# Kernel tuning notes

Measured on AMD Instinct MI355X. Metric: run time of the kernel, lower is better.

## Reference

```python
import jax, jax.numpy as jnp
import numpy as np

# Hypernetwork config (matches init_kwargs)
INP = 4096      # inp_size
MSK = 64        # mask_size
HID = 64        # node_hidden_size (target-net hidden)
OUT = 10        # out_size (target outputs)
L1, L2, L3 = 64, 256, 128  # hypernet trunk layers
B = 16384       # batch
WVEC = MSK * HID + HID + HID * OUT + OUT  # 4810 generated weights per sample


def _linear_params(key, fan_in, fan_out):
    # torch.nn.Linear default init: U(-1/sqrt(fan_in), 1/sqrt(fan_in))
    lim = 1.0 / np.sqrt(fan_in)
    kw, kb = jax.random.split(key)
    W = jax.random.uniform(kw, (fan_out, fan_in), minval=-lim, maxval=lim, dtype=jnp.float32)
    b = jax.random.uniform(kb, (fan_out,), minval=-lim, maxval=lim, dtype=jnp.float32)
    return W, b


def setup_inputs() -> dict:
    key = jax.random.key(0)
    ks = jax.random.split(key, 6)
    W1, b1 = _linear_params(ks[0], INP, L1)
    W2, b2 = _linear_params(ks[1], L1, L2)
    W3, b3 = _linear_params(ks[2], L2, L3)
    W4, b4 = _linear_params(ks[3], L3, WVEC)
    data = jax.random.normal(ks[4], (B, INP), dtype=jnp.float32)
    mask_idx = jnp.sort(jax.random.randint(ks[5], (B, MSK), 0, INP), axis=1)  # int indices of active features
    return dict(data=data, mask_idx=mask_idx,
                W1=W1, b1=b1, W2=W2, b2=b2, W3=W3, b3=b3, W4=W4, b4=b4)


def reference(data, mask_idx, W1, b1, W2, b2, W3, b3, W4, b4):
    b = data.shape[0]
    # Rebuild the float binary mask [B, INP] from indices (scatter ones)
    rows = jnp.arange(b)[:, None]
    mask = jnp.zeros((b, INP), dtype=data.dtype).at[rows, mask_idx].set(1.0)

    # craft_network: 4-layer MLP on the mask (dropout is identity in eval / for reference)
    h = jax.nn.relu(mask @ W1.T + b1)
    h = jax.nn.relu(h @ W2.T + b2)
    h = jax.nn.relu(h @ W3.T + b3)
    w = h @ W4.T + b4  # [B, WVEC] generated weights per sample

    # Split per-sample generated weights (same layout as InsertableNet)
    iw_end = MSK * HID
    ib_end = iw_end + HID
    ow_end = ib_end + HID * OUT
    inp_w = w[:, :iw_end].reshape(b, HID, MSK)       # [B, H, M]
    inp_b = w[:, iw_end:ib_end]                      # [B, H]
    out_w = w[:, ib_end:ow_end].reshape(b, OUT, HID) # [B, O, H]
    out_b = w[:, ow_end:]                            # [B, O]

    # Per-sample gather of masked features: data[i, mask[i]] -> [B, M]
    xm = jnp.take_along_axis(data, mask_idx, axis=1)

    # Batched tiny 2-layer MLP (replaces the per-sample Python loop)
    hid = jax.nn.relu(jnp.einsum('bhm,bm->bh', inp_w, xm) + inp_b)
    res = jnp.einsum('boh,bh->bo', out_w, hid) + out_b  # [B, OUT]
    return res
```

## Files before the change

### kernel.cpp

```cpp
#include <hip/hip_runtime.h>


typedef _Float16 f16;
typedef _Float16 f16x8 __attribute__((ext_vector_type(8)));
typedef _Float16 f16x4 __attribute__((ext_vector_type(4)));
typedef float    f32x4 __attribute__((ext_vector_type(4)));

#define NPAD 4864

__global__ __launch_bounds__(256) void k_prep(
    const float* __restrict__ W1, const float* __restrict__ W2,
    const float* __restrict__ W3, const float* __restrict__ W4,
    f16* __restrict__ W1Th, f16* __restrict__ W2h,
    f16* __restrict__ W3h, f16* __restrict__ W4s)
{
    const int tid = blockIdx.x * 256 + threadIdx.x;
    const int stride = gridDim.x * 256;
    for (int e = tid; e < 4096 * 64; e += stride) {
        int j = e >> 6, i = e & 63;
        W1Th[e] = (f16)W1[(size_t)i * 4096 + j];
    }
    for (int e = tid; e < NPAD * 128; e += stride) {
        const int j    = e & 7;
        const int lane = (e >> 3) & 63;
        const int mt   = (e >> 9) & 3;
        const int kk   = (e >> 11) & 3;
        const int c    = e >> 13;
        const int lr = lane & 15, g = lane >> 4;
        const int row = 64 * c + 16 * mt + lr;
        const int col = 32 * kk + 8 * g + j;
        W4s[e] = (row < 4810) ? (f16)W4[(size_t)row * 128 + col] : (f16)0.f;
    }
    for (int e = tid; e < 256 * 64; e += stride)  W2h[e] = (f16)W2[e];
    for (int e = tid; e < 128 * 256; e += stride) W3h[e] = (f16)W3[e];
}

__global__ __launch_bounds__(512, 2) void k_main(
    const float* __restrict__ data, const int* __restrict__ midx,
    const f16* __restrict__ W1Th, const float* __restrict__ b1,
    const f16* __restrict__ W2h, const float* __restrict__ b2,
    const f16* __restrict__ W3h, const float* __restrict__ b3,
    const f16* __restrict__ W4s, const float* __restrict__ b4,
    float* __restrict__ out)
{
    __shared__ __align__(16) char uMain[65536];
    __shared__ __align__(16) char uB[17408];
    __shared__ __align__(16) char uC[17408];
    __shared__ __align__(16) float b4_s[NPAD];
    __shared__ __align__(16) float res_s[64 * 12];

    const int t = threadIdx.x, w = t >> 6, lane = t & 63;
    const int lr = lane & 15, g = lane >> 4;
    const int sg = w >> 1, cp = w & 1;
    const int row0 = blockIdx.x * 64;
    const f32x4 zero = {0.f, 0.f, 0.f, 0.f};

    int*   idx_s = (int*)uB;
    char*  h2b   = uMain;
    char*  h1b   = uMain + 32768;
    char*  h3b   = uC;
    char*  stage = uMain;
    float* xm_s  = (float*)uB;
    float* hid_s = (float*)uC;

    const char* W4b = (const char*)W4s;
    f32x4 rS0, rS1, rS2, rS3;

    {
        const char* gp = W4b + (size_t)t * 16;
        rS0 = *(const f32x4*)(gp);
        rS1 = *(const f32x4*)(gp + 8192);
        rS2 = *(const f32x4*)(gp + 16384);
        rS3 = *(const f32x4*)(gp + 24576);
    }

    for (int e = t; e < 4096; e += 512)
        idx_s[e] = midx[(size_t)row0 * 64 + e];
    for (int i = t; i < NPAD; i += 512)
        b4_s[i] = (i < 4810) ? b4[i] : 0.f;
    __syncthreads();

    float xr[8];
    #pragma unroll
    for (int k = 0; k < 8; ++k) {
        const int e = k * 512 + t;
        xr[k] = data[(size_t)(row0 + (e >> 6)) * 4096 + idx_s[e]];
    }

    {
        const f32x4 b1v = *(const f32x4*)&b1[lr * 4];
        for (int p = 0; p < 4; ++p) {
            const int s0 = 8 * w + 2 * p, s1 = s0 + 1;
            f32x4 a0 = zero, a1 = zero;
            #pragma unroll
            for (int tt = 0; tt < 16; ++tt) {
                const int i = g * 16 + tt;
                const int c0 = idx_s[s0 * 64 + i];
                const int q0 = (i > 0) ? idx_s[s0 * 64 + i - 1] : -1;
                const int c1 = idx_s[s1 * 64 + i];
                const int q1 = (i > 0) ? idx_s[s1 * 64 + i - 1] : -1;
                const f16x4 w0 = *(const f16x4*)&W1Th[c0 * 64 + lr * 4];
                const f16x4 w1 = *(const f16x4*)&W1Th[c1 * 64 + lr * 4];
                #pragma unroll
                for (int q = 0; q < 4; ++q) {
                    a0[q] += (c0 != q0) ? (float)w0[q] : 0.f;
                    a1[q] += (c1 != q1) ? (float)w1[q] : 0.f;
                }
            }
            #pragma unroll
            for (int q = 0; q < 4; ++q) {
                a0[q] += __shfl_xor(a0[q], 16);
                a0[q] += __shfl_xor(a0[q], 32);
                a1[q] += __shfl_xor(a1[q], 16);
                a1[q] += __shfl_xor(a1[q], 32);
            }
            if (g == 0) {
                f16x4 h0, h1v;
                #pragma unroll
                for (int q = 0; q < 4; ++q) {
                    h0[q]  = (f16)fmaxf(a0[q] + b1v[q], 0.f);
                    h1v[q] = (f16)fmaxf(a1[q] + b1v[q], 0.f);
                }
                *(f16x4*)(h1b + ((s0 * 128 + lr * 8) ^ ((s0 & 7) << 4))) = h0;
                *(f16x4*)(h1b + ((s1 * 128 + lr * 8) ^ ((s1 & 7) << 4))) = h1v;
            }
        }
    }
    __syncthreads();

    {
        f16x8 a2[2][2], bh[4][2];
        #pragma unroll
        for (int mt = 0; mt < 2; ++mt)
            #pragma unroll
            for (int kk = 0; kk < 2; ++kk)
                a2[mt][kk] = *(const f16x8*)&W2h[(32 * w + 16 * mt + lr) * 64 + 32 * kk + 8 * g];
        #pragma unroll
        for (int rt = 0; rt < 4; ++rt)
            #pragma unroll
            for (int kk = 0; kk < 2; ++kk) {
                const int s = 16 * rt + lr;
                bh[rt][kk] = *(const f16x8*)(h1b + ((s * 128 + (32 * kk + 8 * g) * 2) ^ ((s & 7) << 4)));
            }

        f32x4 acc2[2][4];
        #pragma unroll
        for (int mt = 0; mt < 2; ++mt)
            #pragma unroll
            for (int rt = 0; rt < 4; ++rt) {
                acc2[mt][rt] = __builtin_amdgcn_mfma_f32_16x16x32_f16(a2[mt][0], bh[rt][0], zero, 0, 0, 0);
                acc2[mt][rt] = __builtin_amdgcn_mfma_f32_16x16x32_f16(a2[mt][1], bh[rt][1], acc2[mt][rt], 0, 0, 0);
            }

        #pragma unroll
        for (int mt = 0; mt < 2; ++mt) {
            const f32x4 bv = *(const f32x4*)&b2[32 * w + 16 * mt + 4 * g];
            #pragma unroll
            for (int rt = 0; rt < 4; ++rt) {
                const int s = 16 * rt + lr;
                f16x4 hv;
                #pragma unroll
                for (int q = 0; q < 4; ++q)
                    hv[q] = (f16)fmaxf(acc2[mt][rt][q] + bv[q], 0.f);
                *(f16x4*)(h2b + ((s * 512 + (32 * w + 16 * mt + 4 * g) * 2) ^ ((s & 7) << 4))) = hv;
            }
        }
    }
    __syncthreads();

    {
        f32x4 acc3[4] = {zero, zero, zero, zero};
        #pragma unroll 2
        for (int kk = 0; kk < 8; ++kk) {
            const f16x8 a3 = *(const f16x8*)&W3h[(16 * w + lr) * 256 + 32 * kk + 8 * g];
            #pragma unroll
            for (int rt = 0; rt < 4; ++rt) {
                const int s = 16 * rt + lr;
                const f16x8 bb = *(const f16x8*)(h2b + ((s * 512 + (32 * kk + 8 * g) * 2) ^ ((s & 7) << 4)));
                acc3[rt] = __builtin_amdgcn_mfma_f32_16x16x32_f16(a3, bb, acc3[rt], 0, 0, 0);
            }
        }
        const f32x4 bv3 = *(const f32x4*)&b3[16 * w + 4 * g];
        #pragma unroll
        for (int rt = 0; rt < 4; ++rt) {
            const int s = 16 * rt + lr;
            f16x4 hv;
            #pragma unroll
            for (int q = 0; q < 4; ++q)
                hv[q] = (f16)fmaxf(acc3[rt][q] + bv3[q], 0.f);
            *(f16x4*)(h3b + ((s * 256 + (16 * w + 4 * g) * 2) ^ ((s & 7) << 4))) = hv;
        }
    }
    __syncthreads();

    {
        char* lp = stage + t * 16;
        *(f32x4*)(lp)         = rS0;
        *(f32x4*)(lp + 8192)  = rS1;
        *(f32x4*)(lp + 16384) = rS2;
        *(f32x4*)(lp + 24576) = rS3;
    }
    {
        const char* gp = W4b + 32768 + (size_t)t * 16;
        rS0 = *(const f32x4*)(gp);
        rS1 = *(const f32x4*)(gp + 8192);
        rS2 = *(const f32x4*)(gp + 16384);
        rS3 = *(const f32x4*)(gp + 24576);
    }
    #pragma unroll
    for (int k = 0; k < 8; ++k) {
        const int e = k * 512 + t;
        xm_s[(e >> 6) * 68 + (e & 63)] = xr[k];
    }
    const int s = 16 * sg + lr;
    f16x8 bfrag[4];
    #pragma unroll
    for (int kk = 0; kk < 4; ++kk)
        bfrag[kk] = *(const f16x8*)(h3b + ((s * 256 + (32 * kk + 8 * g) * 2) ^ ((s & 7) << 4)));
    __syncthreads();

    f32x4 xmr[4];
    #pragma unroll
    for (int mt = 0; mt < 4; ++mt)
        xmr[mt] = *(const f32x4*)&xm_s[s * 68 + 16 * mt + 4 * g];
    f32x4 hidr[4];

    for (int tp = 0; tp < 38; ++tp) {
        const char* pb = stage + (tp & 1) * 32768;

        if (tp < 32) {
            const int c = 2 * tp + cp;
            const char* cb = pb + (c & 1) * 16384;
            f32x4 acc[4] = {zero, zero, zero, zero};
            #pragma unroll
            for (int kk = 0; kk < 4; ++kk) {
                f16x8 af[4];
                #pragma unroll
                for (int mt = 0; mt < 4; ++mt)
                    af[mt] = *(const f16x8*)(cb + kk * 4096 + mt * 1024 + lane * 16);
                #pragma unroll
                for (int mt = 0; mt < 4; ++mt)
                    acc[mt] = __builtin_amdgcn_mfma_f32_16x16x32_f16(af[mt], bfrag[kk], acc[mt], 0, 0, 0);
            }
            float sum = 0.f;
            #pragma unroll
            for (int mt = 0; mt < 4; ++mt) {
                const f32x4 bv = *(const f32x4*)&b4_s[64 * c + 16 * mt + 4 * g];
                #pragma unroll
                for (int q = 0; q < 4; ++q)
                    sum += (acc[mt][q] + bv[q]) * xmr[mt][q];
            }
            sum += __shfl_xor(sum, 16);
            sum += __shfl_xor(sum, 32);
            if (g == 0) hid_s[s * 68 + c] = sum;
        } else if (tp == 32) {
            f32x4 accb[2] = {zero, zero};
            #pragma unroll
            for (int kk = 0; kk < 4; ++kk) {
                f16x8 af[2];
                #pragma unroll
                for (int i = 0; i < 2; ++i)
                    af[i] = *(const f16x8*)(pb + kk * 4096 + (2 * cp + i) * 1024 + lane * 16);
                #pragma unroll
                for (int i = 0; i < 2; ++i)
                    accb[i] = __builtin_amdgcn_mfma_f32_16x16x32_f16(af[i], bfrag[kk], accb[i], 0, 0, 0);
            }
            #pragma unroll
            for (int i = 0; i < 2; ++i) {
                const int hb = 16 * (2 * cp + i) + 4 * g;
                f32x4 hv = *(const f32x4*)&hid_s[s * 68 + hb];
                const f32x4 bv = *(const f32x4*)&b4_s[4096 + hb];
                #pragma unroll
                for (int q = 0; q < 4; ++q)
                    hv[q] = fmaxf(hv[q] + accb[i][q] + bv[q], 0.f);
                *(f32x4*)&hid_s[s * 68 + hb] = hv;
            }
            __syncthreads();
            #pragma unroll
            for (int mt = 0; mt < 4; ++mt)
                hidr[mt] = *(const f32x4*)&hid_s[s * 68 + 16 * mt + 4 * g];
            if (cp == 0) {
                const char* cb = pb + 16384;
                f32x4 acc[4] = {zero, zero, zero, zero};
                #pragma unroll
                for (int kk = 0; kk < 4; ++kk) {
                    f16x8 af[4];
                    #pragma unroll
                    for (int mt = 0; mt < 4; ++mt)
                        af[mt] = *(const f16x8*)(cb + kk * 4096 + mt * 1024 + lane * 16);
                    #pragma unroll
                    for (int mt = 0; mt < 4; ++mt)
                        acc[mt] = __builtin_amdgcn_mfma_f32_16x16x32_f16(af[mt], bfrag[kk], acc[mt], 0, 0, 0);
                }
                float sum = 0.f;
                #pragma unroll
                for (int mt = 0; mt < 4; ++mt) {
                    const f32x4 bv = *(const f32x4*)&b4_s[4160 + 16 * mt + 4 * g];
                    #pragma unroll
                    for (int q = 0; q < 4; ++q)
                        sum += (acc[mt][q] + bv[q]) * hidr[mt][q];
                }
                sum += __shfl_xor(sum, 16);
                sum += __shfl_xor(sum, 32);
                if (g == 0) res_s[s * 12 + 0] = sum;
            }
        } else {
            const int c = 2 * tp + cp;
            if (c < 75) {
                const char* cb = pb + (c & 1) * 16384;
                f32x4 acc[4] = {zero, zero, zero, zero};
                #pragma unroll
                for (int kk = 0; kk < 4; ++kk) {
                    f16x8 af[4];
                    #pragma unroll
                    for (int mt = 0; mt < 4; ++mt)
                        af[mt] = *(const f16x8*)(cb + kk * 4096 + mt * 1024 + lane * 16);
                    #pragma unroll
                    for (int mt = 0; mt < 4; ++mt)
                        acc[mt] = __builtin_amdgcn_mfma_f32_16x16x32_f16(af[mt], bfrag[kk], acc[mt], 0, 0, 0);
                }
                float sum = 0.f;
                #pragma unroll
                for (int mt = 0; mt < 4; ++mt) {
                    const f32x4 bv = *(const f32x4*)&b4_s[64 * c + 16 * mt + 4 * g];
                    #pragma unroll
                    for (int q = 0; q < 4; ++q)
                        sum += (acc[mt][q] + bv[q]) * hidr[mt][q];
                }
                sum += __shfl_xor(sum, 16);
                sum += __shfl_xor(sum, 32);
                if (g == 0) res_s[s * 12 + (c - 65)] = sum;
            }
        }
        __syncthreads();

        if (tp + 1 < 38) {
            char* lp = stage + ((tp + 1) & 1) * 32768 + t * 16;
            *(f32x4*)(lp)         = rS0;
            *(f32x4*)(lp + 8192)  = rS1;
            *(f32x4*)(lp + 16384) = rS2;
            *(f32x4*)(lp + 24576) = rS3;
            if (tp + 2 < 38) {
                const char* gp = W4b + (size_t)(tp + 2) * 32768 + (size_t)t * 16;
                rS0 = *(const f32x4*)(gp);
                rS1 = *(const f32x4*)(gp + 8192);
                rS2 = *(const f32x4*)(gp + 16384);
                rS3 = *(const f32x4*)(gp + 24576);
            }
            __syncthreads();
        }
    }

    if (cp == 1) {
        const char* cb = stage + 32768 + 16384;
        f32x4 acc = zero;
        #pragma unroll
        for (int kk = 0; kk < 4; ++kk) {
            const f16x8 af = *(const f16x8*)(cb + kk * 4096 + lane * 16);
            acc = __builtin_amdgcn_mfma_f32_16x16x32_f16(af, bfrag[kk], acc, 0, 0, 0);
        }
        #pragma unroll
        for (int q = 0; q < 4; ++q) {
            const int o = 4 * g + q;
            if (o < 10)
                res_s[s * 12 + o] += acc[q] + b4_s[4800 + o];
        }
    }
    __syncthreads();

    for (int e = t; e < 640; e += 512)
        out[(size_t)row0 * 10 + e] = res_s[(e / 10) * 12 + (e % 10)];
}

extern "C" void kernel_launch(void* const* d_in, const int* in_sizes, int n_in,
                              void* d_out, int out_size, void* d_ws, size_t ws_size,
                              hipStream_t stream)
{
    const float* data = (const float*)d_in[0];
    const int*   midx = (const int*)d_in[1];
    const float* W1   = (const float*)d_in[2];
    const float* b1   = (const float*)d_in[3];
    const float* W2   = (const float*)d_in[4];
    const float* b2   = (const float*)d_in[5];
    const float* W3   = (const float*)d_in[6];
    const float* b3   = (const float*)d_in[7];
    const float* W4   = (const float*)d_in[8];
    const float* b4   = (const float*)d_in[9];
    float* out = (float*)d_out;

    f16* W1Th = (f16*)d_ws;
    f16* W4s  = W1Th + (size_t)4096 * 64;
    f16* W2h  = W4s + (size_t)NPAD * 128;
    f16* W3h  = W2h + 256 * 64;

    k_prep<<<512, 256, 0, stream>>>(W1, W2, W3, W4, W1Th, W2h, W3h, W4s);
    k_main<<<256, 512, 0, stream>>>(data, midx, W1Th, b1, W2h, b2, W3h, b3,
                                    W4s, b4, out);
}
```

Before: 81.29 us.

## Load W4 fragments directly from global into registers, dropping LDS staging

The layer-4 phase no longer double-buffers W4 chunks through shared memory with per-step barriers. Each wave now loads A fragments straight from global/L2 in a software-pipelined pattern and computes all four 16-row sample groups at once, holding B fragments for every group in registers. Biases are read from global instead of an LDS copy, and activations are held as f16 to save registers. This removes most __syncthreads and shrinks LDS, which may allow more blocks per CU, but raises register pressure and relies on L2 serving the repeated W4 reads.

```diff
diff --git a/kernel.cpp b/kernel.cpp
--- a/kernel.cpp
+++ b/kernel.cpp
@@ -43,15 +43,13 @@
     const f16* __restrict__ W4s, const float* __restrict__ b4,
     float* __restrict__ out)
 {
-    __shared__ __align__(16) char uMain[65536];
+    __shared__ __align__(16) char uMain[40960];
     __shared__ __align__(16) char uB[17408];
     __shared__ __align__(16) char uC[17408];
-    __shared__ __align__(16) float b4_s[NPAD];
     __shared__ __align__(16) float res_s[64 * 12];
 
     const int t = threadIdx.x, w = t >> 6, lane = t & 63;
     const int lr = lane & 15, g = lane >> 4;
-    const int sg = w >> 1, cp = w & 1;
     const int row0 = blockIdx.x * 64;
     const f32x4 zero = {0.f, 0.f, 0.f, 0.f};
 
@@ -59,25 +57,11 @@
     char*  h2b   = uMain;
     char*  h1b   = uMain + 32768;
     char*  h3b   = uC;
-    char*  stage = uMain;
     float* xm_s  = (float*)uB;
     float* hid_s = (float*)uC;
 
-    const char* W4b = (const char*)W4s;
-    f32x4 rS0, rS1, rS2, rS3;
-
-    {
-        const char* gp = W4b + (size_t)t * 16;
-        rS0 = *(const f32x4*)(gp);
-        rS1 = *(const f32x4*)(gp + 8192);
-        rS2 = *(const f32x4*)(gp + 16384);
-        rS3 = *(const f32x4*)(gp + 24576);
-    }
-
     for (int e = t; e < 4096; e += 512)
         idx_s[e] = midx[(size_t)row0 * 64 + e];
-    for (int i = t; i < NPAD; i += 512)
-        b4_s[i] = (i < 4810) ? b4[i] : 0.f;
     __syncthreads();
 
     float xr[8];
@@ -193,183 +177,189 @@
     }
     __syncthreads();
 
-    {
-        char* lp = stage + t * 16;
-        *(f32x4*)(lp)         = rS0;
-        *(f32x4*)(lp + 8192)  = rS1;
-        *(f32x4*)(lp + 16384) = rS2;
-        *(f32x4*)(lp + 24576) = rS3;
-    }
-    {
-        const char* gp = W4b + 32768 + (size_t)t * 16;
-        rS0 = *(const f32x4*)(gp);
-        rS1 = *(const f32x4*)(gp + 8192);
-        rS2 = *(const f32x4*)(gp + 16384);
-        rS3 = *(const f32x4*)(gp + 24576);
-    }
     #pragma unroll
     for (int k = 0; k < 8; ++k) {
         const int e = k * 512 + t;
         xm_s[(e >> 6) * 68 + (e & 63)] = xr[k];
     }
-    const int s = 16 * sg + lr;
-    f16x8 bfrag[4];
-    #pragma unroll
-    for (int kk = 0; kk < 4; ++kk)
-        bfrag[kk] = *(const f16x8*)(h3b + ((s * 256 + (32 * kk + 8 * g) * 2) ^ ((s & 7) << 4)));
-    __syncthreads();
-
-    f32x4 xmr[4];
+    f16x8 bfrag[4][4];
+    #pragma unroll
+    for (int u = 0; u < 4; ++u)
+        #pragma unroll
+        for (int kk = 0; kk < 4; ++kk) {
+            const int s = 16 * u + lr;
+            bfrag[kk][u] = *(const f16x8*)(h3b + ((s * 256 + (32 * kk + 8 * g) * 2) ^ ((s & 7) << 4)));
+        }
+    __syncthreads();
+
+    f16x4 xmr[4][4];
     #pragma unroll
     for (int mt = 0; mt < 4; ++mt)
-        xmr[mt] = *(const f32x4*)&xm_s[s * 68 + 16 * mt + 4 * g];
-    f32x4 hidr[4];
-
-    for (int tp = 0; tp < 38; ++tp) {
-        const char* pb = stage + (tp & 1) * 32768;
-
-        if (tp < 32) {
-            const int c = 2 * tp + cp;
-            const char* cb = pb + (c & 1) * 16384;
-            f32x4 acc[4] = {zero, zero, zero, zero};
-            #pragma unroll
-            for (int kk = 0; kk < 4; ++kk) {
-                f16x8 af[4];
+        #pragma unroll
+        for (int u = 0; u < 4; ++u) {
+            const f32x4 xv = *(const f32x4*)&xm_s[(16 * u + lr) * 68 + 16 * mt + 4 * g];
+            f16x4 xh;
+            #pragma unroll
+            for (int q = 0; q < 4; ++q) xh[q] = (f16)xv[q];
+            xmr[mt][u] = xh;
+        }
+
+    const char* W4b = (const char*)W4s;
+    const int afoff = lane * 16;
+
+#define LDAF(dst, c, kk) { const char* cb_ = W4b + (size_t)(c) * 16384 + (kk) * 4096 + afoff; \
+    dst[0] = *(const f16x8*)(cb_);        dst[1] = *(const f16x8*)(cb_ + 1024); \
+    dst[2] = *(const f16x8*)(cb_ + 2048); dst[3] = *(const f16x8*)(cb_ + 3072); }
+
+#define MFMA16(af, kk) { \
+    _Pragma("unroll") for (int mt = 0; mt < 4; ++mt) \
+    _Pragma("unroll") for (int u = 0; u < 4; ++u) \
+        acc[mt][u] = __builtin_amdgcn_mfma_f32_16x16x32_f16(af[mt], bfrag[kk][u], acc[mt][u], 0, 0, 0); }
+
+    {
+        f16x8 afA[4], afB[4];
+        LDAF(afA, w, 0)
+        for (int i = 0; i < 8; ++i) {
+            const int c = 8 * i + w;
+            f32x4 bv[4];
+            #pragma unroll
+            for (int mt = 0; mt < 4; ++mt)
+                bv[mt] = *(const f32x4*)&b4[64 * c + 16 * mt + 4 * g];
+            LDAF(afB, c, 1)
+            f32x4 acc[4][4];
+            #pragma unroll
+            for (int mt = 0; mt < 4; ++mt)
+                #pragma unroll
+                for (int u = 0; u < 4; ++u)
+                    acc[mt][u] = __builtin_amdgcn_mfma_f32_16x16x32_f16(afA[mt], bfrag[0][u], zero, 0, 0, 0);
+            LDAF(afA, c, 2)
+            MFMA16(afB, 1)
+            LDAF(afB, c, 3)
+            MFMA16(afA, 2)
+            if (i < 7) { LDAF(afA, 8 * (i + 1) + w, 0) }
+            MFMA16(afB, 3)
+
+            #pragma unroll
+            for (int u = 0; u < 4; ++u) {
+                float sum = 0.f;
                 #pragma unroll
                 for (int mt = 0; mt < 4; ++mt)
-                    af[mt] = *(const f16x8*)(cb + kk * 4096 + mt * 1024 + lane * 16);
-                #pragma unroll
-                for (int mt = 0; mt < 4; ++mt)
-                    acc[mt] = __builtin_amdgcn_mfma_f32_16x16x32_f16(af[mt], bfrag[kk], acc[mt], 0, 0, 0);
-            }
+                    #pragma unroll
+                    for (int q = 0; q < 4; ++q)
+                        sum += (acc[mt][u][q] + bv[mt][q]) * (float)xmr[mt][u][q];
+                sum += __shfl_xor(sum, 16);
+                sum += __shfl_xor(sum, 32);
+                if (g == 0) hid_s[(16 * u + lr) * 68 + c] = sum;
+            }
+        }
+    }
+
+    f32x4 acc64[4] = {zero, zero, zero, zero};
+    if (w < 4) {
+        f16x8 af64[4];
+        #pragma unroll
+        for (int kk = 0; kk < 4; ++kk)
+            af64[kk] = *(const f16x8*)(W4b + (size_t)64 * 16384 + kk * 4096 + w * 1024 + afoff);
+        #pragma unroll
+        for (int kk = 0; kk < 4; ++kk)
+            #pragma unroll
+            for (int u = 0; u < 4; ++u)
+                acc64[u] = __builtin_amdgcn_mfma_f32_16x16x32_f16(af64[kk], bfrag[kk][u], acc64[u], 0, 0, 0);
+    }
+    __syncthreads();
+    if (w < 4) {
+        const f32x4 bv64 = *(const f32x4*)&b4[4096 + 16 * w + 4 * g];
+        #pragma unroll
+        for (int u = 0; u < 4; ++u) {
+            float* hp = &hid_s[(16 * u + lr) * 68 + 16 * w + 4 * g];
+            f32x4 hv = *(const f32x4*)hp;
+            #pragma unroll
+            for (int q = 0; q < 4; ++q)
+                hv[q] = hv[q] + acc64[u][q] + bv64[q];
+            *(f32x4*)hp = hv;
+        }
+    }
+    __syncthreads();
+    for (int e = t; e < 4096; e += 512) {
+        const int si = e >> 6, h = e & 63;
+        hid_s[si * 68 + h] = fmaxf(hid_s[si * 68 + h], 0.f);
+    }
+    __syncthreads();
+    #pragma unroll
+    for (int mt = 0; mt < 4; ++mt)
+        #pragma unroll
+        for (int u = 0; u < 4; ++u) {
+            const f32x4 hv = *(const f32x4*)&hid_s[(16 * u + lr) * 68 + 16 * mt + 4 * g];
+            f16x4 xh;
+            #pragma unroll
+            for (int q = 0; q < 4; ++q) xh[q] = (f16)hv[q];
+            xmr[mt][u] = xh;
+        }
+
+    auto do_out = [&](int c) {
+        f32x4 bv[4];
+        #pragma unroll
+        for (int mt = 0; mt < 4; ++mt)
+            bv[mt] = *(const f32x4*)&b4[64 * c + 16 * mt + 4 * g];
+        f16x8 afA[4], afB[4];
+        LDAF(afA, c, 0)
+        LDAF(afB, c, 1)
+        f32x4 acc[4][4];
+        #pragma unroll
+        for (int mt = 0; mt < 4; ++mt)
+            #pragma unroll
+            for (int u = 0; u < 4; ++u)
+                acc[mt][u] = __builtin_amdgcn_mfma_f32_16x16x32_f16(afA[mt], bfrag[0][u], zero, 0, 0, 0);
+        LDAF(afA, c, 2)
+        MFMA16(afB, 1)
+        LDAF(afB, c, 3)
+        MFMA16(afA, 2)
+        MFMA16(afB, 3)
+        #pragma unroll
+        for (int u = 0; u < 4; ++u) {
             float sum = 0.f;
             #pragma unroll
-            for (int mt = 0; mt < 4; ++mt) {
-                const f32x4 bv = *(const f32x4*)&b4_s[64 * c + 16 * mt + 4 * g];
+            for (int mt = 0; mt < 4; ++mt)
                 #pragma unroll
                 for (int q = 0; q < 4; ++q)
-                    sum += (acc[mt][q] + bv[q]) * xmr[mt][q];
-            }
+                    sum += (acc[mt][u][q] + bv[mt][q]) * (float)xmr[mt][u][q];
             sum += __shfl_xor(sum, 16);
             sum += __shfl_xor(sum, 32);
-            if (g == 0) hid_s[s * 68 + c] = sum;
-        } else if (tp == 32) {
-            f32x4 accb[2] = {zero, zero};
-            #pragma unroll
-            for (int kk = 0; kk < 4; ++kk) {
-                f16x8 af[2];
-                #pragma unroll
-                for (int i = 0; i < 2; ++i)
-                    af[i] = *(const f16x8*)(pb + kk * 4096 + (2 * cp + i) * 1024 + lane * 16);
-                #pragma unroll
-                for (int i = 0; i < 2; ++i)
-                    accb[i] = __builtin_amdgcn_mfma_f32_16x16x32_f16(af[i], bfrag[kk], accb[i], 0, 0, 0);
-            }
-            #pragma unroll
-            for (int i = 0; i < 2; ++i) {
-                const int hb = 16 * (2 * cp + i) + 4 * g;
-                f32x4 hv = *(const f32x4*)&hid_s[s * 68 + hb];
-                const f32x4 bv = *(const f32x4*)&b4_s[4096 + hb];
-                #pragma unroll
-                for (int q = 0; q < 4; ++q)
-                    hv[q] = fmaxf(hv[q] + accb[i][q] + bv[q], 0.f);
-                *(f32x4*)&hid_s[s * 68 + hb] = hv;
-            }
-            __syncthreads();
-            #pragma unroll
-            for (int mt = 0; mt < 4; ++mt)
-                hidr[mt] = *(const f32x4*)&hid_s[s * 68 + 16 * mt + 4 * g];
-            if (cp == 0) {
-                const char* cb = pb + 16384;
-                f32x4 acc[4] = {zero, zero, zero, zero};
-                #pragma unroll
-                for (int kk = 0; kk < 4; ++kk) {
-                    f16x8 af[4];
-                    #pragma unroll
-                    for (int mt = 0; mt < 4; ++mt)
-                        af[mt] = *(const f16x8*)(cb + kk * 4096 + mt * 1024 + lane * 16);
-                    #pragma unroll
-                    for (int mt = 0; mt < 4; ++mt)
-                        acc[mt] = __builtin_amdgcn_mfma_f32_16x16x32_f16(af[mt], bfrag[kk], acc[mt], 0, 0, 0);
-                }
-                float sum = 0.f;
-                #pragma unroll
-                for (int mt = 0; mt < 4; ++mt) {
-                    const f32x4 bv = *(const f32x4*)&b4_s[4160 + 16 * mt + 4 * g];
-                    #pragma unroll
-                    for (int q = 0; q < 4; ++q)
-                        sum += (acc[mt][q] + bv[q]) * hidr[mt][q];
-                }
-                sum += __shfl_xor(sum, 16);
-                sum += __shfl_xor(sum, 32);
-                if (g == 0) res_s[s * 12 + 0] = sum;
-            }
-        } else {
-            const int c = 2 * tp + cp;
-            if (c < 75) {
-                const char* cb = pb + (c & 1) * 16384;
-                f32x4 acc[4] = {zero, zero, zero, zero};
-                #pragma unroll
-                for (int kk = 0; kk < 4; ++kk) {
-                    f16x8 af[4];
-                    #pragma unroll
-                    for (int mt = 0; mt < 4; ++mt)
-                        af[mt] = *(const f16x8*)(cb + kk * 4096 + mt * 1024 + lane * 16);
-                    #pragma unroll
-                    for (int mt = 0; mt < 4; ++mt)
-                        acc[mt] = __builtin_amdgcn_mfma_f32_16x16x32_f16(af[mt], bfrag[kk], acc[mt], 0, 0, 0);
-                }
-                float sum = 0.f;
-                #pragma unroll
-                for (int mt = 0; mt < 4; ++mt) {
-                    const f32x4 bv = *(const f32x4*)&b4_s[64 * c + 16 * mt + 4 * g];
-                    #pragma unroll
-                    for (int q = 0; q < 4; ++q)
-                        sum += (acc[mt][q] + bv[q]) * hidr[mt][q];
-                }
-                sum += __shfl_xor(sum, 16);
-                sum += __shfl_xor(sum, 32);
-                if (g == 0) res_s[s * 12 + (c - 65)] = sum;
-            }
-        }
-        __syncthreads();
-
-        if (tp + 1 < 38) {
-            char* lp = stage + ((tp + 1) & 1) * 32768 + t * 16;
-            *(f32x4*)(lp)         = rS0;
-            *(f32x4*)(lp + 8192)  = rS1;
-            *(f32x4*)(lp + 16384) = rS2;
-            *(f32x4*)(lp + 24576) = rS3;
-            if (tp + 2 < 38) {
-                const char* gp = W4b + (size_t)(tp + 2) * 32768 + (size_t)t * 16;
-                rS0 = *(const f32x4*)(gp);
-                rS1 = *(const f32x4*)(gp + 8192);
-                rS2 = *(const f32x4*)(gp + 16384);
-                rS3 = *(const f32x4*)(gp + 24576);
-            }
-            __syncthreads();
-        }
-    }
-
-    if (cp == 1) {
-        const char* cb = stage + 32768 + 16384;
-        f32x4 acc = zero;
-        #pragma unroll
-        for (int kk = 0; kk < 4; ++kk) {
-            const f16x8 af = *(const f16x8*)(cb + kk * 4096 + lane * 16);
-            acc = __builtin_amdgcn_mfma_f32_16x16x32_f16(af, bfrag[kk], acc, 0, 0, 0);
-        }
-        #pragma unroll
-        for (int q = 0; q < 4; ++q) {
-            const int o = 4 * g + q;
-            if (o < 10)
-                res_s[s * 12 + o] += acc[q] + b4_s[4800 + o];
-        }
+            if (g == 0) res_s[(16 * u + lr) * 12 + (c - 65)] = sum;
+        }
+    };
+    do_out(65 + w);
+    if (w >= 6) do_out(67 + w);
+
+    f32x4 acc75[4] = {zero, zero, zero, zero};
+    if (w == 4) {
+        f16x8 af75[4];
+        #pragma unroll
+        for (int kk = 0; kk < 4; ++kk)
+            af75[kk] = *(const f16x8*)(W4b + (size_t)75 * 16384 + kk * 4096 + afoff);
+        #pragma unroll
+        for (int kk = 0; kk < 4; ++kk)
+            #pragma unroll
+            for (int u = 0; u < 4; ++u)
+                acc75[u] = __builtin_amdgcn_mfma_f32_16x16x32_f16(af75[kk], bfrag[kk][u], acc75[u], 0, 0, 0);
+    }
+    __syncthreads();
+    if (w == 4) {
+        #pragma unroll
+        for (int u = 0; u < 4; ++u)
+            #pragma unroll
+            for (int q = 0; q < 4; ++q) {
+                const int o = 4 * g + q;
+                if (o < 10)
+                    res_s[(16 * u + lr) * 12 + o] += acc75[u][q] + b4[4800 + o];
+            }
     }
     __syncthreads();
 
     for (int e = t; e < 640; e += 512)
         out[(size_t)row0 * 10 + e] = res_s[(e / 10) * 12 + (e % 10)];
+#undef LDAF
+#undef MFMA16
 }
 
 extern "C" void kernel_launch(void* const* d_in, const int* in_sizes, int n_in,
```

Measured after the change: 78.46 us. 1.04x faster.
